# Kernel tuning notes

Measured on AMD Instinct MI355X. Metric: run time of the kernel, lower is better.

## Reference

```python
import jax, jax.numpy as jnp
import numpy as np

T = 128
IN_SIZE = 1024
OUT_SIZE = 1024
LMBDA = 0.01          # lmbda_in_in (also used for out_in update, as in source)
MAX_POST = 1.0
MAX_PRE = 1.0
CONN_SPARSITY = 0.1   # in_in_sparsity / out_in_sparsity


def setup_inputs() -> dict:
    key = jax.random.key(0)
    k1, k2, k3, k4, k5 = jax.random.split(key, 5)
    inputs = jax.random.normal(k1, (T, IN_SIZE), dtype=jnp.float32)
    # fixed weights ~ nn.Linear init (uniform +-1/sqrt(fan_in)) * g * sparse mask
    b_in = 1.0 / np.sqrt(IN_SIZE)
    in_in_fixed = jax.random.uniform(k2, (IN_SIZE, IN_SIZE), jnp.float32, -b_in, b_in)
    in_in_fixed = in_in_fixed * (jax.random.uniform(k3, (IN_SIZE, IN_SIZE)) < CONN_SPARSITY).astype(jnp.float32)
    b_out = 1.0 / np.sqrt(IN_SIZE)
    out_in_fixed = jax.random.uniform(k4, (OUT_SIZE, IN_SIZE), jnp.float32, -b_out, b_out)
    out_in_fixed = out_in_fixed * (jax.random.uniform(k5, (OUT_SIZE, IN_SIZE)) < CONN_SPARSITY).astype(jnp.float32)
    return {"inputs": inputs, "in_in_fixed": in_in_fixed, "out_in_fixed": out_in_fixed}


def _renorm(P, max_post, max_pre):
    # row (post) renorm then column (pre) renorm, only where sums exceed cap
    post = P.sum(axis=1)
    P = P * jnp.where(post > max_post, max_post / post, 1.0)[:, None]
    pre = P.sum(axis=0)
    P = P * jnp.where(pre > max_pre, max_pre / pre, 1.0)[None, :]
    return P


def reference(inputs, in_in_fixed, out_in_fixed):
    def step(carry, x):
        in_in_p, out_in_p = carry
        # forward_input path: out = F.linear(in_, out_in)
        out = (out_in_fixed + out_in_p) @ x                      # [OUT_SIZE]
        # Hebbian outer-product updates + renorm homeostasis
        in_in_p = _renorm(in_in_p + LMBDA * jnp.outer(x, x), MAX_POST, MAX_PRE)
        out_in_p = _renorm(out_in_p + LMBDA * jnp.outer(out, x), MAX_POST, MAX_PRE)
        return (in_in_p, out_in_p), out

    init = (jnp.zeros_like(in_in_fixed), jnp.zeros_like(out_in_fixed))
    (in_in_p, out_in_p), outs = jax.lax.scan(step, init, inputs)
    return outs  # [T, OUT_SIZE]
```

## Files before the change

kernel.cpp:

```cpp
#include <hip/hip_runtime.h>


typedef float f32x4 __attribute__((ext_vector_type(4)));
typedef float f32x2 __attribute__((ext_vector_type(2)));

#define T_STEPS 128
#define N 1024
#define GR 16
#define GC 16
#define TB 64
#define NT 256
#define LMBDA 0.01f

__global__ __launch_bounds__(NT) void rf2d_kernel(
    const float* __restrict__ X,
    const float* __restrict__ W,
    float* __restrict__ OUT,
    f32x2* __restrict__ OutP,
    float* __restrict__ Scol,
    unsigned* __restrict__ fAr, unsigned* __restrict__ fAc,
    unsigned* __restrict__ fBr, unsigned* __restrict__ fBc) {
  __shared__ float Pl[TB * TB];
  __shared__ float f_loc[TB];
  __shared__ float rfl[TB], outll[TB];
  __shared__ float SLc[4][TB];
  __shared__ float sxAll[T_STEPS];

  const int tid = threadIdx.x;
  const int b = blockIdx.x;
  const int r = b >> 4, c = b & 15;
  const int grow = r * TB, gcol = c * TB;

  const int r_loc = tid >> 2, q = tid & 3;
  const int c_loc = tid & 63, rg = tid >> 6;

  for (int i = tid; i < TB * TB; i += NT) Pl[i] = 0.f;
  if (tid < TB) f_loc[tid] = 1.f;
  if (tid < T_STEPS) {
    const f32x4* X4 = (const f32x4*)(X + (size_t)tid * N);
    float a = 0.f;
    for (int j = 0; j < N / 4; ++j) { f32x4 v = X4[j]; a += v.x + v.y + v.z + v.w; }
    sxAll[tid] = a;
  }
  f32x4 wr[4];
#pragma unroll
  for (int k = 0; k < 4; ++k)
    wr[k] = *(const f32x4*)(W + (size_t)(grow + r_loc) * N + gcol + 16 * q + 4 * k);

  __syncthreads();

  for (int t = 0; t < T_STEPS; ++t) {
    const int p = t & 1;
    const unsigned tg = t + 1u;

    float a_out = 0.f, a_R = 0.f;
#pragma unroll
    for (int k = 0; k < 4; ++k) {
      const int chunk = q * 4 + k;
      f32x4 pv = ((const f32x4*)Pl)[r_loc * 16 + (chunk ^ (r_loc & 15))];
      f32x4 fv = ((const f32x4*)f_loc)[chunk];
      f32x4 xv = *(const f32x4*)(X + (size_t)t * N + gcol + 16 * q + 4 * k);
      f32x4 pf = pv * fv;
      a_R += pf.x + pf.y + pf.z + pf.w;
      f32x4 s = (pf + wr[k]) * xv;
      a_out += s.x + s.y + s.z + s.w;
    }
    a_out += __shfl_xor(a_out, 1, 64); a_out += __shfl_xor(a_out, 2, 64);
    a_R   += __shfl_xor(a_R, 1, 64);   a_R   += __shfl_xor(a_R, 2, 64);

    if (q == 0) {
      f32x2 v; v.x = a_out; v.y = a_R;
      f32x2* dst = OutP + ((size_t)p * GC + c) * N + grow + r_loc;
      asm volatile("global_store_dwordx2 %0, %1, off sc0 sc1"
                   :: "v"(dst), "v"(v) : "memory");
    }
    __syncthreads();
    if (tid == 0) {
      __hip_atomic_store(&fAr[r * GC + c], tg, __ATOMIC_RELAXED, __HIP_MEMORY_SCOPE_AGENT);
      __hip_atomic_store(&fAc[c * GR + r], tg, __ATOMIC_RELAXED, __HIP_MEMORY_SCOPE_AGENT);
    }
    if (tid < 32) {
      const unsigned* pp = (tid < 16) ? &fAr[r * GC + tid] : &fAc[c * GR + (tid - 16)];
      while (__hip_atomic_load(pp, __ATOMIC_RELAXED, __HIP_MEMORY_SCOPE_AGENT) < tg)
        __builtin_amdgcn_s_sleep(1);
    }
    __syncthreads();

    {
      const f32x2* base = OutP + (size_t)p * GC * N + grow + r_loc;
      f32x2 vv[4];
#pragma unroll
      for (int i = 0; i < 4; ++i) {
        const f32x2* ap = base + (size_t)(4 * q + i) * N;
        asm volatile("global_load_dwordx2 %0, %1, off sc0 sc1"
                     : "=v"(vv[i]) : "v"(ap) : "memory");
      }
      asm volatile("s_waitcnt vmcnt(0)" ::: "memory");
      __builtin_amdgcn_sched_barrier(0);
      f32x2 s2 = (vv[0] + vv[1]) + (vv[2] + vv[3]);
      s2.x += __shfl_xor(s2.x, 1, 64); s2.x += __shfl_xor(s2.x, 2, 64);
      s2.y += __shfl_xor(s2.y, 1, 64); s2.y += __shfl_xor(s2.y, 2, 64);
      float out = s2.x;
      float ol = LMBDA * out;
      float R1 = s2.y + ol * sxAll[t];
      float rf = (R1 > 1.f) ? 1.f / R1 : 1.f;
      if (q == 0) { rfl[r_loc] = rf; outll[r_loc] = ol; }
      if (c == 0 && q == 0) OUT[(size_t)t * N + grow + r_loc] = out;
    }
    if (t == T_STEPS - 1) break;
    __syncthreads();

    {
      const float xc = X[(size_t)t * N + gcol + c_loc];
      const float fc = f_loc[c_loc];
      float cacc = 0.f;
#pragma unroll
      for (int rr = 0; rr < 16; ++rr) {
        const int row = rg * 16 + rr;
        const int idx = row * 64 + ((((c_loc >> 2) ^ (row & 15))) << 2) + (c_loc & 3);
        float v = rfl[row] * (Pl[idx] * fc + outll[row] * xc);
        Pl[idx] = v;
        cacc += v;
      }
      SLc[rg][c_loc] = cacc;
    }
    __syncthreads();

    if (tid < TB) {
      float scol = (SLc[0][tid] + SLc[1][tid]) + (SLc[2][tid] + SLc[3][tid]);
      float* dst = Scol + ((size_t)p * GR + r) * N + gcol + tid;
      asm volatile("global_store_dword %0, %1, off sc0 sc1"
                   :: "v"(dst), "v"(scol) : "memory");
    }
    __syncthreads();
    if (tid == 0) {
      __hip_atomic_store(&fBr[r * GC + c], tg, __ATOMIC_RELAXED, __HIP_MEMORY_SCOPE_AGENT);
      __hip_atomic_store(&fBc[c * GR + r], tg, __ATOMIC_RELAXED, __HIP_MEMORY_SCOPE_AGENT);
    }
    if (tid < 32) {
      const unsigned* pp = (tid < 16) ? &fBr[r * GC + tid] : &fBc[c * GR + (tid - 16)];
      while (__hip_atomic_load(pp, __ATOMIC_RELAXED, __HIP_MEMORY_SCOPE_AGENT) < tg)
        __builtin_amdgcn_s_sleep(1);
    }
    __syncthreads();

    {
      const float* base = Scol + (size_t)p * GR * N + gcol + c_loc;
      float vv[4];
#pragma unroll
      for (int i = 0; i < 4; ++i) {
        const float* ap = base + (size_t)(4 * rg + i) * N;
        asm volatile("global_load_dword %0, %1, off sc0 sc1"
                     : "=v"(vv[i]) : "v"(ap) : "memory");
      }
      asm volatile("s_waitcnt vmcnt(0)" ::: "memory");
      __builtin_amdgcn_sched_barrier(0);
      SLc[rg][c_loc] = (vv[0] + vv[1]) + (vv[2] + vv[3]);
    }
    __syncthreads();
    if (tid < TB) {
      float s = (SLc[0][tid] + SLc[1][tid]) + (SLc[2][tid] + SLc[3][tid]);
      f_loc[tid] = (s > 1.f) ? 1.f / s : 1.f;
    }
    __syncthreads();
  }
}

extern "C" void kernel_launch(void* const* d_in, const int* in_sizes, int n_in,
                              void* d_out, int out_size, void* d_ws, size_t ws_size,
                              hipStream_t stream) {
  const float* X = (const float*)d_in[0];
  const float* W = (const float*)d_in[2];
  float* OUT = (float*)d_out;

  char* ws = (char*)d_ws;
  unsigned* fAr = (unsigned*)ws;
  unsigned* fAc = fAr + 256;
  unsigned* fBr = fAc + 256;
  unsigned* fBc = fBr + 256;
  f32x2* OutP = (f32x2*)(ws + 4096);
  float* Scol = (float*)(ws + 4096 + (size_t)2 * GC * N * 8);

  hipMemsetAsync(ws, 0, 4096, stream);

  hipLaunchKernelGGL(rf2d_kernel, dim3(GR * GC), dim3(NT), 0, stream,
                     X, W, OUT, OutP, Scol, fAr, fAc, fBr, fBc);
}
```

Before: 634.1 us.

## Replace flag barriers with tagged data exchange and deferred buffer-reuse flags

Partial sums exchanged between blocks now carry a step tag in the same vector store, so readers spin on the data itself instead of a separate flag write plus a flag poll. The remaining flags only guard reuse of the double-buffered slots and are checked one or two steps late, which takes them off the critical path. The column renorm factor is folded into P at the start of each step, the fixed-weight dot product with the next input is precomputed off the critical path, and the update is reorganised as rf*P + rf*ol*x. This cuts two grid-wide barrier round trips per step, at the cost of wider stores, spin loads over the data region, and more subtle memory-ordering assumptions.

```diff
diff --git a/kernel.cpp b/kernel.cpp
--- a/kernel.cpp
+++ b/kernel.cpp
@@ -16,151 +16,193 @@
     const float* __restrict__ X,
     const float* __restrict__ W,
     float* __restrict__ OUT,
-    f32x2* __restrict__ OutP,
-    float* __restrict__ Scol,
-    unsigned* __restrict__ fAr, unsigned* __restrict__ fAc,
-    unsigned* __restrict__ fBr, unsigned* __restrict__ fBc) {
+    f32x4* __restrict__ OutA,
+    f32x2* __restrict__ ScolB,
+    unsigned* __restrict__ fAr,
+    unsigned* __restrict__ fBc) {
   __shared__ float Pl[TB * TB];
   __shared__ float f_loc[TB];
-  __shared__ float rfl[TB], outll[TB];
+  __shared__ float rfl[TB], rol_l[TB];
   __shared__ float SLc[4][TB];
+  __shared__ float SLd[4][TB];
   __shared__ float sxAll[T_STEPS];
 
   const int tid = threadIdx.x;
   const int b = blockIdx.x;
   const int r = b >> 4, c = b & 15;
   const int grow = r * TB, gcol = c * TB;
-
   const int r_loc = tid >> 2, q = tid & 3;
   const int c_loc = tid & 63, rg = tid >> 6;
 
   for (int i = tid; i < TB * TB; i += NT) Pl[i] = 0.f;
   if (tid < TB) f_loc[tid] = 1.f;
   if (tid < T_STEPS) {
-    const f32x4* X4 = (const f32x4*)(X + (size_t)tid * N);
-    float a = 0.f;
-    for (int j = 0; j < N / 4; ++j) { f32x4 v = X4[j]; a += v.x + v.y + v.z + v.w; }
-    sxAll[tid] = a;
+    const f32x4* X4i = (const f32x4*)(X + (size_t)tid * N);
+    f32x4 acc = {0.f, 0.f, 0.f, 0.f};
+    for (int j = 0; j < N / 4; ++j) acc += X4i[j];
+    sxAll[tid] = (acc.x + acc.y) + (acc.z + acc.w);
   }
   f32x4 wr[4];
 #pragma unroll
   for (int k = 0; k < 4; ++k)
     wr[k] = *(const f32x4*)(W + (size_t)(grow + r_loc) * N + gcol + 16 * q + 4 * k);
 
+  float wrx = 0.f;
+  {
+    const f32x4* Xn = (const f32x4*)(X + gcol);
+#pragma unroll
+    for (int k = 0; k < 4; ++k) {
+      f32x4 xv = Xn[4 * q + k];
+      wrx += (wr[k].x * xv.x + wr[k].y * xv.y) + (wr[k].z * xv.z + wr[k].w * xv.w);
+    }
+  }
   __syncthreads();
 
   for (int t = 0; t < T_STEPS; ++t) {
     const int p = t & 1;
     const unsigned tg = t + 1u;
-
-    float a_out = 0.f, a_R = 0.f;
-#pragma unroll
-    for (int k = 0; k < 4; ++k) {
-      const int chunk = q * 4 + k;
-      f32x4 pv = ((const f32x4*)Pl)[r_loc * 16 + (chunk ^ (r_loc & 15))];
-      f32x4 fv = ((const f32x4*)f_loc)[chunk];
-      f32x4 xv = *(const f32x4*)(X + (size_t)t * N + gcol + 16 * q + 4 * k);
-      f32x4 pf = pv * fv;
-      a_R += pf.x + pf.y + pf.z + pf.w;
-      f32x4 s = (pf + wr[k]) * xv;
-      a_out += s.x + s.y + s.z + s.w;
+    const float tagf = __uint_as_float(tg);
+
+    float a_out = wrx, a_R = 0.f;
+    {
+      f32x4* PlV = (f32x4*)Pl;
+      const f32x4* FV = (const f32x4*)f_loc;
+      const f32x4* XV = (const f32x4*)(X + (size_t)t * N + gcol);
+#pragma unroll
+      for (int k = 0; k < 4; ++k) {
+        const int lc = 4 * q + k;
+        const int slot = r_loc * 16 + (lc ^ (r_loc & 15));
+        f32x4 pv = PlV[slot];
+        f32x4 fv = FV[lc];
+        f32x4 xv = XV[lc];
+        f32x4 pf = pv * fv;
+        PlV[slot] = pf;
+        a_R += (pf.x + pf.y) + (pf.z + pf.w);
+        a_out += (pf.x * xv.x + pf.y * xv.y) + (pf.z * xv.z + pf.w * xv.w);
+      }
     }
     a_out += __shfl_xor(a_out, 1, 64); a_out += __shfl_xor(a_out, 2, 64);
     a_R   += __shfl_xor(a_R, 1, 64);   a_R   += __shfl_xor(a_R, 2, 64);
 
     if (q == 0) {
-      f32x2 v; v.x = a_out; v.y = a_R;
-      f32x2* dst = OutP + ((size_t)p * GC + c) * N + grow + r_loc;
-      asm volatile("global_store_dwordx2 %0, %1, off sc0 sc1"
+      f32x4 v; v.x = a_out; v.y = a_R; v.z = tagf; v.w = 0.f;
+      f32x4* dst = OutA + (size_t)p * GC * N + (size_t)c * N + grow + r_loc;
+      asm volatile("global_store_dwordx4 %0, %1, off sc0 sc1"
                    :: "v"(dst), "v"(v) : "memory");
     }
-    __syncthreads();
-    if (tid == 0) {
+
+    f32x4 v0, v1, v2, v3;
+    {
+      const f32x4* baseA = OutA + (size_t)p * GC * N + grow + r_loc;
+      for (;;) {
+        asm volatile("global_load_dwordx4 %0, %4, off sc0 sc1\n\t"
+                     "global_load_dwordx4 %1, %5, off sc0 sc1\n\t"
+                     "global_load_dwordx4 %2, %6, off sc0 sc1\n\t"
+                     "global_load_dwordx4 %3, %7, off sc0 sc1\n\t"
+                     "s_waitcnt vmcnt(0)"
+                     : "=v"(v0), "=v"(v1), "=v"(v2), "=v"(v3)
+                     : "v"(baseA + (size_t)(4 * q + 0) * N),
+                       "v"(baseA + (size_t)(4 * q + 1) * N),
+                       "v"(baseA + (size_t)(4 * q + 2) * N),
+                       "v"(baseA + (size_t)(4 * q + 3) * N)
+                     : "memory");
+        __builtin_amdgcn_sched_barrier(0);
+        if (__float_as_uint(v0.z) == tg && __float_as_uint(v1.z) == tg &&
+            __float_as_uint(v2.z) == tg && __float_as_uint(v3.z) == tg)
+          break;
+      }
+    }
+    {
+      float po = (v0.x + v1.x) + (v2.x + v3.x);
+      float pR = (v0.y + v1.y) + (v2.y + v3.y);
+      po += __shfl_xor(po, 1, 64); po += __shfl_xor(po, 2, 64);
+      pR += __shfl_xor(pR, 1, 64); pR += __shfl_xor(pR, 2, 64);
+      float ol = LMBDA * po;
+      float R1 = pR + ol * sxAll[t];
+      float rf = (R1 > 1.f) ? 1.f / R1 : 1.f;
+      if (q == 0) { rfl[r_loc] = rf; rol_l[r_loc] = rf * ol; }
+      if (c == 0 && q == 0) OUT[(size_t)t * N + grow + r_loc] = po;
+    }
+    if (t == T_STEPS - 1) break;
+    __syncthreads();
+
+    if (tid == 0)
       __hip_atomic_store(&fAr[r * GC + c], tg, __ATOMIC_RELAXED, __HIP_MEMORY_SCOPE_AGENT);
-      __hip_atomic_store(&fAc[c * GR + r], tg, __ATOMIC_RELAXED, __HIP_MEMORY_SCOPE_AGENT);
-    }
-    if (tid < 32) {
-      const unsigned* pp = (tid < 16) ? &fAr[r * GC + tid] : &fAc[c * GR + (tid - 16)];
-      while (__hip_atomic_load(pp, __ATOMIC_RELAXED, __HIP_MEMORY_SCOPE_AGENT) < tg)
-        __builtin_amdgcn_s_sleep(1);
-    }
-    __syncthreads();
-
-    {
-      const f32x2* base = OutP + (size_t)p * GC * N + grow + r_loc;
-      f32x2 vv[4];
-#pragma unroll
-      for (int i = 0; i < 4; ++i) {
-        const f32x2* ap = base + (size_t)(4 * q + i) * N;
-        asm volatile("global_load_dwordx2 %0, %1, off sc0 sc1"
-                     : "=v"(vv[i]) : "v"(ap) : "memory");
-      }
-      asm volatile("s_waitcnt vmcnt(0)" ::: "memory");
-      __builtin_amdgcn_sched_barrier(0);
-      f32x2 s2 = (vv[0] + vv[1]) + (vv[2] + vv[3]);
-      s2.x += __shfl_xor(s2.x, 1, 64); s2.x += __shfl_xor(s2.x, 2, 64);
-      s2.y += __shfl_xor(s2.y, 1, 64); s2.y += __shfl_xor(s2.y, 2, 64);
-      float out = s2.x;
-      float ol = LMBDA * out;
-      float R1 = s2.y + ol * sxAll[t];
-      float rf = (R1 > 1.f) ? 1.f / R1 : 1.f;
-      if (q == 0) { rfl[r_loc] = rf; outll[r_loc] = ol; }
-      if (c == 0 && q == 0) OUT[(size_t)t * N + grow + r_loc] = out;
-    }
-    if (t == T_STEPS - 1) break;
-    __syncthreads();
 
     {
       const float xc = X[(size_t)t * N + gcol + c_loc];
-      const float fc = f_loc[c_loc];
       float cacc = 0.f;
 #pragma unroll
       for (int rr = 0; rr < 16; ++rr) {
         const int row = rg * 16 + rr;
         const int idx = row * 64 + ((((c_loc >> 2) ^ (row & 15))) << 2) + (c_loc & 3);
-        float v = rfl[row] * (Pl[idx] * fc + outll[row] * xc);
+        float v = rfl[row] * Pl[idx] + rol_l[row] * xc;
         Pl[idx] = v;
         cacc += v;
       }
       SLc[rg][c_loc] = cacc;
     }
+    if (tid < 16 && (int)t >= 2) {
+      const unsigned tgt = t - 1u;
+      while (__hip_atomic_load(&fBc[c * GR + tid], __ATOMIC_RELAXED,
+                               __HIP_MEMORY_SCOPE_AGENT) < tgt)
+        __builtin_amdgcn_s_sleep(1);
+    }
     __syncthreads();
 
     if (tid < TB) {
       float scol = (SLc[0][tid] + SLc[1][tid]) + (SLc[2][tid] + SLc[3][tid]);
-      float* dst = Scol + ((size_t)p * GR + r) * N + gcol + tid;
-      asm volatile("global_store_dword %0, %1, off sc0 sc1"
-                   :: "v"(dst), "v"(scol) : "memory");
-    }
-    __syncthreads();
-    if (tid == 0) {
-      __hip_atomic_store(&fBr[r * GC + c], tg, __ATOMIC_RELAXED, __HIP_MEMORY_SCOPE_AGENT);
+      f32x2 v; v.x = scol; v.y = tagf;
+      f32x2* dst = ScolB + (size_t)p * GR * N + (size_t)r * N + gcol + tid;
+      asm volatile("global_store_dwordx2 %0, %1, off sc0 sc1"
+                   :: "v"(dst), "v"(v) : "memory");
+    }
+
+    wrx = 0.f;
+    {
+      const f32x4* Xn = (const f32x4*)(X + (size_t)(t + 1) * N + gcol);
+#pragma unroll
+      for (int k = 0; k < 4; ++k) {
+        f32x4 xv = Xn[4 * q + k];
+        wrx += (wr[k].x * xv.x + wr[k].y * xv.y) + (wr[k].z * xv.z + wr[k].w * xv.w);
+      }
+    }
+
+    {
+      f32x2 u0, u1, u2, u3;
+      const f32x2* baseB = ScolB + (size_t)p * GR * N + gcol + c_loc;
+      for (;;) {
+        asm volatile("global_load_dwordx2 %0, %4, off sc0 sc1\n\t"
+                     "global_load_dwordx2 %1, %5, off sc0 sc1\n\t"
+                     "global_load_dwordx2 %2, %6, off sc0 sc1\n\t"
+                     "global_load_dwordx2 %3, %7, off sc0 sc1\n\t"
+                     "s_waitcnt vmcnt(0)"
+                     : "=v"(u0), "=v"(u1), "=v"(u2), "=v"(u3)
+                     : "v"(baseB + (size_t)(4 * rg + 0) * N),
+                       "v"(baseB + (size_t)(4 * rg + 1) * N),
+                       "v"(baseB + (size_t)(4 * rg + 2) * N),
+                       "v"(baseB + (size_t)(4 * rg + 3) * N)
+                     : "memory");
+        __builtin_amdgcn_sched_barrier(0);
+        if (__float_as_uint(u0.y) == tg && __float_as_uint(u1.y) == tg &&
+            __float_as_uint(u2.y) == tg && __float_as_uint(u3.y) == tg)
+          break;
+      }
+      SLd[rg][c_loc] = (u0.x + u1.x) + (u2.x + u3.x);
+    }
+    __syncthreads();
+
+    if (tid == 0)
       __hip_atomic_store(&fBc[c * GR + r], tg, __ATOMIC_RELAXED, __HIP_MEMORY_SCOPE_AGENT);
-    }
-    if (tid < 32) {
-      const unsigned* pp = (tid < 16) ? &fBr[r * GC + tid] : &fBc[c * GR + (tid - 16)];
-      while (__hip_atomic_load(pp, __ATOMIC_RELAXED, __HIP_MEMORY_SCOPE_AGENT) < tg)
+    if (tid < TB) {
+      float s = (SLd[0][tid] + SLd[1][tid]) + (SLd[2][tid] + SLd[3][tid]);
+      f_loc[tid] = (s > 1.f) ? 1.f / s : 1.f;
+    }
+    if (tid >= 16 && tid < 32 && t >= 1) {
+      const unsigned tgt = t;
+      while (__hip_atomic_load(&fAr[r * GC + (tid - 16)], __ATOMIC_RELAXED,
+                               __HIP_MEMORY_SCOPE_AGENT) < tgt)
         __builtin_amdgcn_s_sleep(1);
-    }
-    __syncthreads();
-
-    {
-      const float* base = Scol + (size_t)p * GR * N + gcol + c_loc;
-      float vv[4];
-#pragma unroll
-      for (int i = 0; i < 4; ++i) {
-        const float* ap = base + (size_t)(4 * rg + i) * N;
-        asm volatile("global_load_dword %0, %1, off sc0 sc1"
-                     : "=v"(vv[i]) : "v"(ap) : "memory");
-      }
-      asm volatile("s_waitcnt vmcnt(0)" ::: "memory");
-      __builtin_amdgcn_sched_barrier(0);
-      SLc[rg][c_loc] = (vv[0] + vv[1]) + (vv[2] + vv[3]);
-    }
-    __syncthreads();
-    if (tid < TB) {
-      float s = (SLc[0][tid] + SLc[1][tid]) + (SLc[2][tid] + SLc[3][tid]);
-      f_loc[tid] = (s > 1.f) ? 1.f / s : 1.f;
     }
     __syncthreads();
   }
@@ -175,14 +217,12 @@
 
   char* ws = (char*)d_ws;
   unsigned* fAr = (unsigned*)ws;
-  unsigned* fAc = fAr + 256;
-  unsigned* fBr = fAc + 256;
-  unsigned* fBc = fBr + 256;
-  f32x2* OutP = (f32x2*)(ws + 4096);
-  float* Scol = (float*)(ws + 4096 + (size_t)2 * GC * N * 8);
-
-  hipMemsetAsync(ws, 0, 4096, stream);
+  unsigned* fBc = (unsigned*)(ws + 1024);
+  f32x4* OutA = (f32x4*)(ws + 4096);
+  f32x2* ScolB = (f32x2*)(ws + 4096 + (size_t)2 * GC * N * sizeof(f32x4));
+
+  hipMemsetAsync(ws, 0, 2048, stream);
 
   hipLaunchKernelGGL(rf2d_kernel, dim3(GR * GC), dim3(NT), 0, stream,
-                     X, W, OUT, OutP, Scol, fAr, fAc, fBr, fBc);
+                     X, W, OUT, OutA, ScolB, fAr, fBc);
 }
```

Result: slower. 743.7 us (+17.3%).
